# Performance work log

Measured on AMD Instinct MI355X. Metric: run time of the kernel, lower is better.

Reference implementation:

```python
import jax, jax.numpy as jnp
import numpy as np

N_NODES = 50000
N_EDGES = 800000
C_IN = 64
C_OUT = 64
K = 3


def setup_inputs() -> dict:
    key = jax.random.key(0)
    k1, k2, k3, k4, k5, k6 = jax.random.split(key, 6)
    x = jax.random.normal(k1, (N_NODES, C_IN), dtype=jnp.float32)
    edge_index = jax.random.randint(k2, (2, N_EDGES), 0, N_NODES, dtype=jnp.int32)
    edge_weight = jax.random.uniform(k3, (N_EDGES,), dtype=jnp.float32)
    # Xavier-uniform init for [K, C_IN, C_OUT] (fan over last two dims)
    limit = float(np.sqrt(6.0 / (C_IN + C_OUT)))
    theta_forward = jax.random.uniform(k4, (K, C_IN, C_OUT), minval=-limit, maxval=limit, dtype=jnp.float32)
    theta_backward = jax.random.uniform(k5, (K, C_IN, C_OUT), minval=-limit, maxval=limit, dtype=jnp.float32)
    return {
        "x": x,
        "edge_index": edge_index,
        "edge_weight": edge_weight,
        "theta_forward": theta_forward,
        "theta_backward": theta_backward,
    }


def _propagate(x, row, col, edge_weight, n_nodes):
    # degree normalization: deg[i] = sum of edge_weight over edges with row == i
    deg = jax.ops.segment_sum(edge_weight, row, num_segments=n_nodes)
    deg_inv = jnp.where(deg > 0, jax.lax.rsqrt(jnp.where(deg > 0, deg, 1.0)), 0.0)
    norm = deg_inv[row] * edge_weight * deg_inv[col]      # [E]
    msg = norm[:, None] * x[col]                          # [E, C] gather-scale
    return jax.ops.segment_sum(msg, row, num_segments=n_nodes)  # scatter-add -> [N, C]


def reference(x, edge_index, edge_weight, theta_forward, theta_backward):
    row, col = edge_index[0], edge_index[1]
    n_nodes = x.shape[0]
    k = theta_forward.shape[0]
    Tx_0 = x
    Tx_1 = _propagate(x, row, col, edge_weight, n_nodes)
    out = Tx_0 @ theta_forward[0] + Tx_1 @ theta_backward[0]
    for i in range(1, k):
        Tx_2 = _propagate(Tx_1, row, col, edge_weight, n_nodes)
        out = out + Tx_2 @ theta_forward[i] + Tx_1 @ theta_backward[i]
        Tx_1 = Tx_2
    return out
```

## Files before the change

### kernel.cpp

```cpp
#include <hip/hip_runtime.h>
#include <hip/hip_fp16.h>


#define N_NODES 50000
#define N_EDGES 800000
#define C 64
#define CAP 64
#define NPART 196
#define CAPP 4608
#define EPB 8192
#define NEB 98
#define XH_BLOCKS 782
#define CW_BLOCKS 16

typedef _Float16 half8 __attribute__((ext_vector_type(8)));
typedef float f32x4 __attribute__((ext_vector_type(4)));

__global__ __launch_bounds__(1024) void scatter2_kernel(
        const int* __restrict__ row, const int* __restrict__ col,
        const float* __restrict__ w, int* __restrict__ percur,
        uint2* __restrict__ pedges,
        const float* __restrict__ x, __half* __restrict__ xh,
        const float* __restrict__ tf, const float* __restrict__ tb,
        _Float16* __restrict__ whc) {
    const int tid = threadIdx.x;
    if (blockIdx.x >= NEB + XH_BLOCKS) {
        int idx = (blockIdx.x - NEB - XH_BLOCKS) * 1024 + tid;
        int j = idx >> 12;
        int rem = idx & 4095;
        int ci = rem >> 6;
        int co = rem & 63;
        float v;
        if (j == 0)      v = tf[rem];
        else if (j == 1) v = tb[rem] + tb[4096 + rem];
        else if (j == 2) v = tf[4096 + rem] + tb[8192 + rem];
        else             v = tf[8192 + rem];
        whc[(j << 12) + (co << 6) + ci] = (_Float16)v;
        return;
    }
    if (blockIdx.x >= NEB) {
        int i = (blockIdx.x - NEB) * 1024 + tid;
        if (i < N_NODES * C / 4) {
            float4 v = ((const float4*)x)[i];
            union { float2 f2; __half2 h2[2]; } u;
            u.h2[0] = __floats2half2_rn(v.x, v.y);
            u.h2[1] = __floats2half2_rn(v.z, v.w);
            ((float2*)xh)[i] = u.f2;
        }
        return;
    }
    __shared__ int h[NPART];
    __shared__ int cur[NPART];
    uint2 ent[8];
    int pp[8];
    if (tid < NPART) h[tid] = 0;
    __syncthreads();
    int base = blockIdx.x * EPB;
#pragma unroll
    for (int i = 0; i < 8; ++i) {
        int e = base + i * 1024 + tid;
        pp[i] = -1;
        if (e < N_EDGES) {
            int r = row[e];
            unsigned int c = (unsigned int)col[e];
            unsigned int wh = (unsigned int)__half_as_ushort(__float2half_rn(w[e]));
            ent[i] = make_uint2((c << 16) | wh, (unsigned int)(r & 255));
            pp[i] = r >> 8;
            atomicAdd(&h[pp[i]], 1);
        }
    }
    __syncthreads();
    if (tid < NPART) cur[tid] = atomicAdd(&percur[tid], h[tid]);
    __syncthreads();
#pragma unroll
    for (int i = 0; i < 8; ++i) {
        if (pp[i] >= 0) {
            int slot = atomicAdd(&cur[pp[i]], 1);
            pedges[(size_t)pp[i] * CAPP + slot] = ent[i];
        }
    }
}

__global__ __launch_bounds__(1024) void build_kernel(
        const uint2* __restrict__ pedges, const int* __restrict__ percur,
        unsigned int* __restrict__ bkt, int* __restrict__ cnt,
        float* __restrict__ dinv) {
    __shared__ unsigned int lbuck[256 * CAP];
    __shared__ int lcnt[256];
    const int tid = threadIdx.x;
    const int p = blockIdx.x;
    if (tid < 256) lcnt[tid] = 0;
    __syncthreads();
    int e = min(percur[p], CAPP);
    const uint2* src = pedges + (size_t)p * CAPP;
    for (int i = tid; i < e; i += 1024) {
        uint2 en = src[i];
        int rl = (int)en.y;
        int slot = atomicAdd(&lcnt[rl], 1);
        if (slot < CAP) lbuck[(rl << 6) + slot] = en.x;
    }
    __syncthreads();
    if (tid < 256) {
        int m = min(lcnt[tid], CAP);
        int g = (p << 8) + tid;
        float sum = 0.f;
        for (int j = 0; j < m; ++j)
            sum += __half2float(__ushort_as_half(
                (unsigned short)(lbuck[(tid << 6) + j] & 0xFFFFu)));
        if (g < N_NODES) {
            cnt[g] = m;
            dinv[g] = (sum > 0.f) ? rsqrtf(sum) : 0.f;
        }
    }
    __syncthreads();
    const uint4* s4 = (const uint4*)lbuck;
    uint4* dst = (uint4*)(bkt + ((size_t)p << 14));
    for (int i = tid; i < 256 * CAP / 4; i += 1024) dst[i] = s4[i];
}

__global__ __launch_bounds__(256) void prop_kernel(
        const __half* __restrict__ xin, __half* __restrict__ xout,
        const int* __restrict__ cnt, const unsigned int* __restrict__ bkt,
        const float* __restrict__ dinv) {
    int wave = (blockIdx.x * blockDim.x + threadIdx.x) >> 6;
    int lane = threadIdx.x & 63;
    int q = lane >> 4;
    int ql = lane & 15;
    int node = (wave << 2) + q;
    if (node >= N_NODES) return;
    int m = min(cnt[node], CAP);
    int base = node << 6;
    int cj[4];
    float nj[4];
#pragma unroll
    for (int s = 0; s < 4; ++s) {
        int idx = (s << 4) + ql;
        cj[s] = 0;
        nj[s] = 0.f;
        if (idx < m) {
            unsigned int b = bkt[base + idx];
            int c = (int)(b >> 16);
            cj[s] = c << 6;
            nj[s] = __half2float(__ushort_as_half((unsigned short)(b & 0xFFFFu))) * dinv[c];
        }
    }
    float ax = 0.f, ay = 0.f, az = 0.f, aw = 0.f;
#pragma unroll
    for (int s = 0; s < 4; ++s) {
        int cb = s << 4;
        if (cb >= m) break;
        int rem = m - cb;
        if (rem > 16) rem = 16;
        int mm = (rem + 7) & ~7;
        for (int jo = 0; jo < mm; jo += 8) {
            int cs[8];
            float ns[8];
            float2 vs[8];
#pragma unroll
            for (int t = 0; t < 8; ++t) {
                cs[t] = __shfl(cj[s], (q << 4) + jo + t);
                ns[t] = __shfl(nj[s], (q << 4) + jo + t);
            }
#pragma unroll
            for (int t = 0; t < 8; ++t)
                vs[t] = *(const float2*)(xin + cs[t] + (ql << 2));
#pragma unroll
            for (int t = 0; t < 8; ++t) {
                const __half2* hp = (const __half2*)&vs[t];
                float2 a = __half22float2(hp[0]);
                float2 b = __half22float2(hp[1]);
                ax += ns[t] * a.x;
                ay += ns[t] * a.y;
                az += ns[t] * b.x;
                aw += ns[t] * b.y;
            }
        }
    }
    float dr = dinv[node];
    union { float2 f2; __half2 h2[2]; } u;
    u.h2[0] = __floats2half2_rn(dr * ax, dr * ay);
    u.h2[1] = __floats2half2_rn(dr * az, dr * aw);
    *(float2*)(xout + base + (ql << 2)) = u.f2;
}

__global__ __launch_bounds__(256) void gemm_mfma_kernel(
        const __half* __restrict__ x0, const __half* __restrict__ x1,
        const __half* __restrict__ x2, const __half* __restrict__ x3,
        const _Float16* __restrict__ whc, float* __restrict__ out) {
    const int tid = threadIdx.x;
    const int wv = tid >> 6;
    const int lane = tid & 63;
    const int quad = lane >> 4;
    const int l16 = lane & 15;
    const int mbase = (blockIdx.x << 6) + (wv << 4);
    const __half* srcs[4] = {x0, x1, x2, x3};
    f32x4 acc0 = {}, acc1 = {}, acc2 = {}, acc3 = {};
    const int arow = mbase + l16;
    const bool aok = arow < N_NODES;
    const size_t abase = ((size_t)arow << 6) + (quad << 3);
    const half8 zero8 = {};
#pragma unroll
    for (int j = 0; j < 4; ++j) {
        const __half* src = srcs[j];
#pragma unroll
        for (int kk = 0; kk < 64; kk += 32) {
            half8 af = aok ? *(const half8*)(const void*)(src + abase + kk) : zero8;
            const _Float16* wb = whc + (j << 12) + kk + (quad << 3);
            half8 b0 = *(const half8*)(const void*)(wb + ((0 * 16 + l16) << 6));
            half8 b1 = *(const half8*)(const void*)(wb + ((1 * 16 + l16) << 6));
            half8 b2 = *(const half8*)(const void*)(wb + ((2 * 16 + l16) << 6));
            half8 b3 = *(const half8*)(const void*)(wb + ((3 * 16 + l16) << 6));
            acc0 = __builtin_amdgcn_mfma_f32_16x16x32_f16(af, b0, acc0, 0, 0, 0);
            acc1 = __builtin_amdgcn_mfma_f32_16x16x32_f16(af, b1, acc1, 0, 0, 0);
            acc2 = __builtin_amdgcn_mfma_f32_16x16x32_f16(af, b2, acc2, 0, 0, 0);
            acc3 = __builtin_amdgcn_mfma_f32_16x16x32_f16(af, b3, acc3, 0, 0, 0);
        }
    }
#pragma unroll
    for (int i = 0; i < 4; ++i) {
        int r = mbase + (quad << 2) + i;
        if (r < N_NODES) {
            float* dst = out + ((size_t)r << 6) + l16;
            dst[0]  = acc0[i];
            dst[16] = acc1[i];
            dst[32] = acc2[i];
            dst[48] = acc3[i];
        }
    }
}

extern "C" void kernel_launch(void* const* d_in, const int* in_sizes, int n_in,
                              void* d_out, int out_size, void* d_ws, size_t ws_size,
                              hipStream_t stream) {
    const float* x  = (const float*)d_in[0];
    const int*   ei = (const int*)d_in[1];
    const float* ew = (const float*)d_in[2];
    const float* tf = (const float*)d_in[3];
    const float* tb = (const float*)d_in[4];
    float* out = (float*)d_out;

    const int* row = ei;
    const int* col = ei + N_EDGES;

    const int NROWS_PAD = NPART * 256;
    float* ws = (float*)d_ws;
    size_t off = 0;
    int*    percur = (int*)(ws + off); off += 256;
    uint2*  pedges = (uint2*)(ws + off); off += (size_t)NPART * CAPP * 2;
    unsigned int* bkt = (unsigned int*)(ws + off); off += (size_t)NROWS_PAD * CAP;
    int*    cnt  = (int*)(ws + off); off += NROWS_PAD;
    float*  dinv = ws + off; off += NROWS_PAD;
    __half* xh   = (__half*)(ws + off); off += (size_t)N_NODES * C / 2;
    __half* tA   = (__half*)(ws + off); off += (size_t)N_NODES * C / 2;
    __half* tB   = (__half*)(ws + off); off += (size_t)N_NODES * C / 2;
    __half* tC   = (__half*)(ws + off); off += (size_t)N_NODES * C / 2;
    _Float16* whc = (_Float16*)(ws + off); off += 4 * 64 * 64 / 2;

    hipMemsetAsync(percur, 0, NPART * sizeof(int), stream);

    scatter2_kernel<<<NEB + XH_BLOCKS + CW_BLOCKS, 1024, 0, stream>>>(
        row, col, ew, percur, pedges, x, xh, tf, tb, whc);
    build_kernel<<<NPART, 1024, 0, stream>>>(pedges, percur, bkt, cnt, dinv);

    const int PB = (N_NODES + 15) / 16;
    prop_kernel<<<PB, 256, 0, stream>>>(xh, tA, cnt, bkt, dinv);
    prop_kernel<<<PB, 256, 0, stream>>>(tA, tB, cnt, bkt, dinv);
    prop_kernel<<<PB, 256, 0, stream>>>(tB, tC, cnt, bkt, dinv);

    const int GB = (N_NODES + 63) / 64;
    gemm_mfma_kernel<<<GB, 256, 0, stream>>>(xh, tA, tB, tC, whc, out);
}
```

Baseline: 165.2 us.

## Fuse last propagation into GEMM and widen gather to 8 nodes per wave

The prop kernel now assigns 8 lanes per node, so each lane loads 16 bytes (8 halfs) per neighbor instead of 8 bytes, and a wave covers 8 nodes instead of 4. The third propagation is folded into the GEMM kernel: each block gathers its 64 rows of Tx3 into shared memory and feeds them straight to MFMA. This drops one launch and the write and reread of the tC buffer. In exchange, the GEMM block does more serial gather work before its MFMAs can start, and each lane needs more registers for the wider loads.

```diff
diff --git a/kernel.cpp b/kernel.cpp
--- a/kernel.cpp
+++ b/kernel.cpp
@@ -118,23 +118,16 @@
     for (int i = tid; i < 256 * CAP / 4; i += 1024) dst[i] = s4[i];
 }
 
-__global__ __launch_bounds__(256) void prop_kernel(
-        const __half* __restrict__ xin, __half* __restrict__ xout,
-        const int* __restrict__ cnt, const unsigned int* __restrict__ bkt,
-        const float* __restrict__ dinv) {
-    int wave = (blockIdx.x * blockDim.x + threadIdx.x) >> 6;
-    int lane = threadIdx.x & 63;
-    int q = lane >> 4;
-    int ql = lane & 15;
-    int node = (wave << 2) + q;
-    if (node >= N_NODES) return;
-    int m = min(cnt[node], CAP);
+__device__ __forceinline__ void gather_row8(
+        const __half* __restrict__ xin, const unsigned int* __restrict__ bkt,
+        const float* __restrict__ dinv, int node, int m, int oct, int ol,
+        float* acc) {
     int base = node << 6;
-    int cj[4];
-    float nj[4];
-#pragma unroll
-    for (int s = 0; s < 4; ++s) {
-        int idx = (s << 4) + ql;
+    int cj[8];
+    float nj[8];
+#pragma unroll
+    for (int s = 0; s < 8; ++s) {
+        int idx = (s << 3) + ol;
         cj[s] = 0;
         nj[s] = 0.f;
         if (idx < m) {
@@ -144,63 +137,97 @@
             nj[s] = __half2float(__ushort_as_half((unsigned short)(b & 0xFFFFu))) * dinv[c];
         }
     }
-    float ax = 0.f, ay = 0.f, az = 0.f, aw = 0.f;
-#pragma unroll
-    for (int s = 0; s < 4; ++s) {
-        int cb = s << 4;
-        if (cb >= m) break;
-        int rem = m - cb;
-        if (rem > 16) rem = 16;
-        int mm = (rem + 7) & ~7;
-        for (int jo = 0; jo < mm; jo += 8) {
-            int cs[8];
-            float ns[8];
-            float2 vs[8];
-#pragma unroll
-            for (int t = 0; t < 8; ++t) {
-                cs[t] = __shfl(cj[s], (q << 4) + jo + t);
-                ns[t] = __shfl(nj[s], (q << 4) + jo + t);
+#pragma unroll
+    for (int s = 0; s < 8; ++s) {
+        if ((s << 3) >= m) break;
+        int cs[8];
+        float ns[8];
+        float4 vs[8];
+#pragma unroll
+        for (int t = 0; t < 8; ++t) {
+            cs[t] = __shfl(cj[s], (oct << 3) + t);
+            ns[t] = __shfl(nj[s], (oct << 3) + t);
+        }
+#pragma unroll
+        for (int t = 0; t < 8; ++t)
+            vs[t] = *(const float4*)(xin + cs[t] + (ol << 3));
+#pragma unroll
+        for (int t = 0; t < 8; ++t) {
+            const __half2* hp = (const __half2*)&vs[t];
+#pragma unroll
+            for (int k = 0; k < 4; ++k) {
+                float2 f = __half22float2(hp[k]);
+                acc[2 * k]     += ns[t] * f.x;
+                acc[2 * k + 1] += ns[t] * f.y;
             }
-#pragma unroll
-            for (int t = 0; t < 8; ++t)
-                vs[t] = *(const float2*)(xin + cs[t] + (ql << 2));
-#pragma unroll
-            for (int t = 0; t < 8; ++t) {
-                const __half2* hp = (const __half2*)&vs[t];
-                float2 a = __half22float2(hp[0]);
-                float2 b = __half22float2(hp[1]);
-                ax += ns[t] * a.x;
-                ay += ns[t] * a.y;
-                az += ns[t] * b.x;
-                aw += ns[t] * b.y;
-            }
-        }
-    }
+        }
+    }
+}
+
+__global__ __launch_bounds__(256) void prop_kernel(
+        const __half* __restrict__ xin, __half* __restrict__ xout,
+        const int* __restrict__ cnt, const unsigned int* __restrict__ bkt,
+        const float* __restrict__ dinv) {
+    int wave = (blockIdx.x * blockDim.x + threadIdx.x) >> 6;
+    int lane = threadIdx.x & 63;
+    int oct = lane >> 3;
+    int ol = lane & 7;
+    int node = (wave << 3) + oct;
+    if (node >= N_NODES) return;
+    int m = min(cnt[node], CAP);
+    float acc[8] = {0.f, 0.f, 0.f, 0.f, 0.f, 0.f, 0.f, 0.f};
+    gather_row8(xin, bkt, dinv, node, m, oct, ol, acc);
     float dr = dinv[node];
-    union { float2 f2; __half2 h2[2]; } u;
-    u.h2[0] = __floats2half2_rn(dr * ax, dr * ay);
-    u.h2[1] = __floats2half2_rn(dr * az, dr * aw);
-    *(float2*)(xout + base + (ql << 2)) = u.f2;
-}
-
-__global__ __launch_bounds__(256) void gemm_mfma_kernel(
+    union { float4 f4; __half2 h2[4]; } u;
+#pragma unroll
+    for (int k = 0; k < 4; ++k)
+        u.h2[k] = __floats2half2_rn(dr * acc[2 * k], dr * acc[2 * k + 1]);
+    *(float4*)(xout + ((size_t)node << 6) + (ol << 3)) = u.f4;
+}
+
+__global__ __launch_bounds__(256) void gemm_fused_kernel(
         const __half* __restrict__ x0, const __half* __restrict__ x1,
-        const __half* __restrict__ x2, const __half* __restrict__ x3,
+        const __half* __restrict__ x2,
+        const int* __restrict__ cnt, const unsigned int* __restrict__ bkt,
+        const float* __restrict__ dinv,
         const _Float16* __restrict__ whc, float* __restrict__ out) {
+    __shared__ _Float16 tCs[64][72];
     const int tid = threadIdx.x;
     const int wv = tid >> 6;
     const int lane = tid & 63;
+    const int oct = lane >> 3;
+    const int ol = lane & 7;
+    const int nb = blockIdx.x << 6;
+#pragma unroll
+    for (int p = 0; p < 2; ++p) {
+        int lrow = (p << 5) + (wv << 3) + oct;
+        int node = nb + lrow;
+        union { float4 f4; __half2 h2[4]; } u;
+        if (node < N_NODES) {
+            int m = min(cnt[node], CAP);
+            float acc[8] = {0.f, 0.f, 0.f, 0.f, 0.f, 0.f, 0.f, 0.f};
+            gather_row8(x2, bkt, dinv, node, m, oct, ol, acc);
+            float dr = dinv[node];
+#pragma unroll
+            for (int k = 0; k < 4; ++k)
+                u.h2[k] = __floats2half2_rn(dr * acc[2 * k], dr * acc[2 * k + 1]);
+        } else {
+            u.f4 = make_float4(0.f, 0.f, 0.f, 0.f);
+        }
+        *(float4*)&tCs[lrow][ol << 3] = u.f4;
+    }
+    __syncthreads();
     const int quad = lane >> 4;
     const int l16 = lane & 15;
-    const int mbase = (blockIdx.x << 6) + (wv << 4);
-    const __half* srcs[4] = {x0, x1, x2, x3};
+    const int mbase = nb + (wv << 4);
+    const __half* srcs[3] = {x0, x1, x2};
     f32x4 acc0 = {}, acc1 = {}, acc2 = {}, acc3 = {};
     const int arow = mbase + l16;
     const bool aok = arow < N_NODES;
     const size_t abase = ((size_t)arow << 6) + (quad << 3);
     const half8 zero8 = {};
 #pragma unroll
-    for (int j = 0; j < 4; ++j) {
+    for (int j = 0; j < 3; ++j) {
         const __half* src = srcs[j];
 #pragma unroll
         for (int kk = 0; kk < 64; kk += 32) {
@@ -217,6 +244,19 @@
         }
     }
 #pragma unroll
+    for (int kk = 0; kk < 64; kk += 32) {
+        half8 af = *(const half8*)&tCs[(wv << 4) + l16][kk + (quad << 3)];
+        const _Float16* wb = whc + (3 << 12) + kk + (quad << 3);
+        half8 b0 = *(const half8*)(const void*)(wb + ((0 * 16 + l16) << 6));
+        half8 b1 = *(const half8*)(const void*)(wb + ((1 * 16 + l16) << 6));
+        half8 b2 = *(const half8*)(const void*)(wb + ((2 * 16 + l16) << 6));
+        half8 b3 = *(const half8*)(const void*)(wb + ((3 * 16 + l16) << 6));
+        acc0 = __builtin_amdgcn_mfma_f32_16x16x32_f16(af, b0, acc0, 0, 0, 0);
+        acc1 = __builtin_amdgcn_mfma_f32_16x16x32_f16(af, b1, acc1, 0, 0, 0);
+        acc2 = __builtin_amdgcn_mfma_f32_16x16x32_f16(af, b2, acc2, 0, 0, 0);
+        acc3 = __builtin_amdgcn_mfma_f32_16x16x32_f16(af, b3, acc3, 0, 0, 0);
+    }
+#pragma unroll
     for (int i = 0; i < 4; ++i) {
         int r = mbase + (quad << 2) + i;
         if (r < N_NODES) {
@@ -253,7 +293,6 @@
     __half* xh   = (__half*)(ws + off); off += (size_t)N_NODES * C / 2;
     __half* tA   = (__half*)(ws + off); off += (size_t)N_NODES * C / 2;
     __half* tB   = (__half*)(ws + off); off += (size_t)N_NODES * C / 2;
-    __half* tC   = (__half*)(ws + off); off += (size_t)N_NODES * C / 2;
     _Float16* whc = (_Float16*)(ws + off); off += 4 * 64 * 64 / 2;
 
     hipMemsetAsync(percur, 0, NPART * sizeof(int), stream);
@@ -262,11 +301,11 @@
         row, col, ew, percur, pedges, x, xh, tf, tb, whc);
     build_kernel<<<NPART, 1024, 0, stream>>>(pedges, percur, bkt, cnt, dinv);
 
-    const int PB = (N_NODES + 15) / 16;
+    const int PB = (N_NODES + 31) / 32;
     prop_kernel<<<PB, 256, 0, stream>>>(xh, tA, cnt, bkt, dinv);
     prop_kernel<<<PB, 256, 0, stream>>>(tA, tB, cnt, bkt, dinv);
-    prop_kernel<<<PB, 256, 0, stream>>>(tB, tC, cnt, bkt, dinv);
 
     const int GB = (N_NODES + 63) / 64;
-    gemm_mfma_kernel<<<GB, 256, 0, stream>>>(xh, tA, tB, tC, whc, out);
-}
+    gemm_fused_kernel<<<GB, 256, 0, stream>>>(
+        xh, tA, tB, cnt, bkt, dinv, whc, out);
+}
```

Result: slower. 170.6 us (+3.3%).

## Fuse third propagation into the MFMA GEMM via shared-memory tile

Applied to the files above, without the earlier changes.

The third sparse propagation is folded into the final GEMM kernel. Each 64-node block gathers its propagated rows straight into a padded LDS tile and feeds that tile to the last MFMA stage, so the tC buffer is never written to or read back from global memory and one launch goes away. The cost is that the GEMM kernel now carries the irregular gather work, with only 782 blocks of 4 waves each, which may lower occupancy and latency hiding compared with the standalone prop kernel.

```diff
diff --git a/kernel.cpp b/kernel.cpp
--- a/kernel.cpp
+++ b/kernel.cpp
@@ -118,6 +118,58 @@
     for (int i = tid; i < 256 * CAP / 4; i += 1024) dst[i] = s4[i];
 }
 
+__device__ __forceinline__ void gather_row4(
+        const __half* __restrict__ xin, const unsigned int* __restrict__ bkt,
+        const float* __restrict__ dinv, int node, int m, int q, int ql,
+        float& ax, float& ay, float& az, float& aw) {
+    int base = node << 6;
+    int cj[4];
+    float nj[4];
+#pragma unroll
+    for (int s = 0; s < 4; ++s) {
+        int idx = (s << 4) + ql;
+        cj[s] = 0;
+        nj[s] = 0.f;
+        if (idx < m) {
+            unsigned int b = bkt[base + idx];
+            int c = (int)(b >> 16);
+            cj[s] = c << 6;
+            nj[s] = __half2float(__ushort_as_half((unsigned short)(b & 0xFFFFu))) * dinv[c];
+        }
+    }
+#pragma unroll
+    for (int s = 0; s < 4; ++s) {
+        int cb = s << 4;
+        if (cb >= m) break;
+        int rem = m - cb;
+        if (rem > 16) rem = 16;
+        int mm = (rem + 7) & ~7;
+        for (int jo = 0; jo < mm; jo += 8) {
+            int cs[8];
+            float ns[8];
+            float2 vs[8];
+#pragma unroll
+            for (int t = 0; t < 8; ++t) {
+                cs[t] = __shfl(cj[s], (q << 4) + jo + t);
+                ns[t] = __shfl(nj[s], (q << 4) + jo + t);
+            }
+#pragma unroll
+            for (int t = 0; t < 8; ++t)
+                vs[t] = *(const float2*)(xin + cs[t] + (ql << 2));
+#pragma unroll
+            for (int t = 0; t < 8; ++t) {
+                const __half2* hp = (const __half2*)&vs[t];
+                float2 a = __half22float2(hp[0]);
+                float2 b = __half22float2(hp[1]);
+                ax += ns[t] * a.x;
+                ay += ns[t] * a.y;
+                az += ns[t] * b.x;
+                aw += ns[t] * b.y;
+            }
+        }
+    }
+}
+
 __global__ __launch_bounds__(256) void prop_kernel(
         const __half* __restrict__ xin, __half* __restrict__ xout,
         const int* __restrict__ cnt, const unsigned int* __restrict__ bkt,
@@ -129,78 +181,56 @@
     int node = (wave << 2) + q;
     if (node >= N_NODES) return;
     int m = min(cnt[node], CAP);
-    int base = node << 6;
-    int cj[4];
-    float nj[4];
-#pragma unroll
-    for (int s = 0; s < 4; ++s) {
-        int idx = (s << 4) + ql;
-        cj[s] = 0;
-        nj[s] = 0.f;
-        if (idx < m) {
-            unsigned int b = bkt[base + idx];
-            int c = (int)(b >> 16);
-            cj[s] = c << 6;
-            nj[s] = __half2float(__ushort_as_half((unsigned short)(b & 0xFFFFu))) * dinv[c];
-        }
-    }
     float ax = 0.f, ay = 0.f, az = 0.f, aw = 0.f;
-#pragma unroll
-    for (int s = 0; s < 4; ++s) {
-        int cb = s << 4;
-        if (cb >= m) break;
-        int rem = m - cb;
-        if (rem > 16) rem = 16;
-        int mm = (rem + 7) & ~7;
-        for (int jo = 0; jo < mm; jo += 8) {
-            int cs[8];
-            float ns[8];
-            float2 vs[8];
-#pragma unroll
-            for (int t = 0; t < 8; ++t) {
-                cs[t] = __shfl(cj[s], (q << 4) + jo + t);
-                ns[t] = __shfl(nj[s], (q << 4) + jo + t);
-            }
-#pragma unroll
-            for (int t = 0; t < 8; ++t)
-                vs[t] = *(const float2*)(xin + cs[t] + (ql << 2));
-#pragma unroll
-            for (int t = 0; t < 8; ++t) {
-                const __half2* hp = (const __half2*)&vs[t];
-                float2 a = __half22float2(hp[0]);
-                float2 b = __half22float2(hp[1]);
-                ax += ns[t] * a.x;
-                ay += ns[t] * a.y;
-                az += ns[t] * b.x;
-                aw += ns[t] * b.y;
-            }
-        }
-    }
+    gather_row4(xin, bkt, dinv, node, m, q, ql, ax, ay, az, aw);
     float dr = dinv[node];
     union { float2 f2; __half2 h2[2]; } u;
     u.h2[0] = __floats2half2_rn(dr * ax, dr * ay);
     u.h2[1] = __floats2half2_rn(dr * az, dr * aw);
-    *(float2*)(xout + base + (ql << 2)) = u.f2;
-}
-
-__global__ __launch_bounds__(256) void gemm_mfma_kernel(
+    *(float2*)(xout + ((size_t)node << 6) + (ql << 2)) = u.f2;
+}
+
+__global__ __launch_bounds__(256) void gemm_fused_kernel(
         const __half* __restrict__ x0, const __half* __restrict__ x1,
-        const __half* __restrict__ x2, const __half* __restrict__ x3,
+        const __half* __restrict__ x2,
+        const int* __restrict__ cnt, const unsigned int* __restrict__ bkt,
+        const float* __restrict__ dinv,
         const _Float16* __restrict__ whc, float* __restrict__ out) {
+    __shared__ _Float16 tCs[64][72];
     const int tid = threadIdx.x;
     const int wv = tid >> 6;
     const int lane = tid & 63;
+    const int q = lane >> 4;
+    const int ql = lane & 15;
+    const int nb = blockIdx.x << 6;
+#pragma unroll
+    for (int p = 0; p < 4; ++p) {
+        int lrow = (p << 4) + (wv << 2) + q;
+        int node = nb + lrow;
+        float ax = 0.f, ay = 0.f, az = 0.f, aw = 0.f;
+        float dr = 0.f;
+        if (node < N_NODES) {
+            int m = min(cnt[node], CAP);
+            gather_row4(x2, bkt, dinv, node, m, q, ql, ax, ay, az, aw);
+            dr = dinv[node];
+        }
+        union { float2 f2; __half2 h2[2]; } u;
+        u.h2[0] = __floats2half2_rn(dr * ax, dr * ay);
+        u.h2[1] = __floats2half2_rn(dr * az, dr * aw);
+        *(float2*)&tCs[lrow][ql << 2] = u.f2;
+    }
+    __syncthreads();
     const int quad = lane >> 4;
     const int l16 = lane & 15;
-    const int mbase = (blockIdx.x << 6) + (wv << 4);
-    const __half* srcs[4] = {x0, x1, x2, x3};
+    const int mbase = nb + (wv << 4);
+    const __half* srcs[3] = {x0, x1, x2};
     f32x4 acc0 = {}, acc1 = {}, acc2 = {}, acc3 = {};
     const int arow = mbase + l16;
     const bool aok = arow < N_NODES;
     const size_t abase = ((size_t)arow << 6) + (quad << 3);
     const half8 zero8 = {};
 #pragma unroll
-    for (int j = 0; j < 4; ++j) {
+    for (int j = 0; j < 3; ++j) {
         const __half* src = srcs[j];
 #pragma unroll
         for (int kk = 0; kk < 64; kk += 32) {
@@ -217,6 +247,19 @@
         }
     }
 #pragma unroll
+    for (int kk = 0; kk < 64; kk += 32) {
+        half8 af = *(const half8*)&tCs[(wv << 4) + l16][kk + (quad << 3)];
+        const _Float16* wb = whc + (3 << 12) + kk + (quad << 3);
+        half8 b0 = *(const half8*)(const void*)(wb + ((0 * 16 + l16) << 6));
+        half8 b1 = *(const half8*)(const void*)(wb + ((1 * 16 + l16) << 6));
+        half8 b2 = *(const half8*)(const void*)(wb + ((2 * 16 + l16) << 6));
+        half8 b3 = *(const half8*)(const void*)(wb + ((3 * 16 + l16) << 6));
+        acc0 = __builtin_amdgcn_mfma_f32_16x16x32_f16(af, b0, acc0, 0, 0, 0);
+        acc1 = __builtin_amdgcn_mfma_f32_16x16x32_f16(af, b1, acc1, 0, 0, 0);
+        acc2 = __builtin_amdgcn_mfma_f32_16x16x32_f16(af, b2, acc2, 0, 0, 0);
+        acc3 = __builtin_amdgcn_mfma_f32_16x16x32_f16(af, b3, acc3, 0, 0, 0);
+    }
+#pragma unroll
     for (int i = 0; i < 4; ++i) {
         int r = mbase + (quad << 2) + i;
         if (r < N_NODES) {
@@ -253,7 +296,6 @@
     __half* xh   = (__half*)(ws + off); off += (size_t)N_NODES * C / 2;
     __half* tA   = (__half*)(ws + off); off += (size_t)N_NODES * C / 2;
     __half* tB   = (__half*)(ws + off); off += (size_t)N_NODES * C / 2;
-    __half* tC   = (__half*)(ws + off); off += (size_t)N_NODES * C / 2;
     _Float16* whc = (_Float16*)(ws + off); off += 4 * 64 * 64 / 2;
 
     hipMemsetAsync(percur, 0, NPART * sizeof(int), stream);
@@ -265,8 +307,8 @@
     const int PB = (N_NODES + 15) / 16;
     prop_kernel<<<PB, 256, 0, stream>>>(xh, tA, cnt, bkt, dinv);
     prop_kernel<<<PB, 256, 0, stream>>>(tA, tB, cnt, bkt, dinv);
-    prop_kernel<<<PB, 256, 0, stream>>>(tB, tC, cnt, bkt, dinv);
 
     const int GB = (N_NODES + 63) / 64;
-    gemm_mfma_kernel<<<GB, 256, 0, stream>>>(xh, tA, tB, tC, whc, out);
-}
+    gemm_fused_kernel<<<GB, 256, 0, stream>>>(
+        xh, tA, tB, cnt, bkt, dinv, whc, out);
+}
```

Measured after the change: 165.3 us. Within noise of the previous version (+0.0%).
